# Optimization experiments

Hardware: AMD Instinct MI355X
Metric: run time of the kernel (lower is better)

## Reference

```python
import jax, jax.numpy as jnp
import numpy as np

N, E = 50000, 800000
IN_F, HID, OUT_F, K = 128, 128, 64, 3
LAMBDA_MAX = 2.0  # standard upper bound for normalized-Laplacian eigenvalues (dgl.laplacian_lambda_max)
BN_EPS = 1e-5


def setup_inputs() -> dict:
    key = jax.random.key(0)
    ks = jax.random.split(key, 8)
    s = 0.05
    features = jax.random.normal(ks[0], (N, IN_F), jnp.float32)
    src = jax.random.randint(ks[1], (E,), 0, N)
    dst = jax.random.randint(ks[2], (E,), 0, N)
    W1 = jax.random.normal(ks[3], (HID, K * IN_F), jnp.float32) * s
    b1 = jnp.zeros((HID,), jnp.float32)
    W3 = jax.random.normal(ks[4], (HID, K * HID), jnp.float32) * s
    b3 = jnp.zeros((HID,), jnp.float32)
    gamma = jnp.ones((HID,), jnp.float32)
    beta = jnp.zeros((HID,), jnp.float32)
    Wm1 = jax.random.normal(ks[5], (HID, HID), jnp.float32) * s
    bm1 = jnp.zeros((HID,), jnp.float32)
    Wm2 = jax.random.normal(ks[6], (OUT_F, HID), jnp.float32) * s
    bm2 = jnp.zeros((OUT_F,), jnp.float32)
    return dict(features=features, src=src, dst=dst, W1=W1, b1=b1, W3=W3, b3=b3,
                gamma=gamma, beta=beta, Wm1=Wm1, bm1=bm1, Wm2=Wm2, bm2=bm2)


def chebconv(feat, src, dst, d_invsqrt, W, b, k):
    """DGL ChebConv: T_0 = X, T_1 = Lhat X, T_i = 2 Lhat T_{i-1} - T_{i-2};
    Lhat = (2/lam) (I - Ahat) - I, Ahat = D^{-1/2} A D^{-1/2}; linear over concat of orders."""
    re_norm = 2.0 / LAMBDA_MAX
    n = feat.shape[0]

    def spmv(x):  # Ahat @ x via edge gather (src) + segment-sum scatter (dst)
        return jax.ops.segment_sum((x * d_invsqrt)[src], dst, num_segments=n) * d_invsqrt

    Xs = [feat]
    if k > 1:
        h = spmv(feat)
        Xs.append(-re_norm * h + feat * (re_norm - 1.0))
    for _ in range(2, k):
        h = spmv(Xs[-1])
        Xs.append(-2.0 * re_norm * h + Xs[-1] * (2.0 * (re_norm - 1.0)) - Xs[-2])
    return jnp.concatenate(Xs, axis=1) @ W.T + b  # [N, k*d] @ [d_out, k*d]^T


def reference(features, src, dst, W1, b1, W3, b3, gamma, beta, Wm1, bm1, Wm2, bm2):
    n = features.shape[0]
    in_deg = jax.ops.segment_sum(jnp.ones((src.shape[0],), jnp.float32), dst, num_segments=n)
    d_invsqrt = (jnp.clip(in_deg, 1.0, None) ** -0.5)[:, None]

    x = jax.nn.relu(chebconv(features, src, dst, d_invsqrt, W1, b1, K))
    # BatchNorm1d (training-mode batch stats, biased variance)
    mu = x.mean(axis=0)
    var = x.var(axis=0)
    x = (x - mu) * jax.lax.rsqrt(var + BN_EPS) * gamma + beta
    # NOTE: the source's Chebyshev early-stopping loop computes cheb2(x) repeatedly but
    # never reassigns `x`, so it is output-inert and omitted (same math).
    x_res = x
    x = jax.nn.relu(chebconv(x, src, dst, d_invsqrt, W3, b3, K))
    x = x + x_res  # dropout in eval mode == identity
    h = jax.nn.relu(x @ Wm1.T + bm1)
    return h @ Wm2.T + bm2
```

## Files before the change

### kernel.cpp

```cpp
#include <hip/hip_runtime.h>
#include <hip/hip_bf16.h>
#include <math.h>

#define NF 128

typedef __bf16 bf16x8 __attribute__((ext_vector_type(8)));
typedef unsigned short ushort8 __attribute__((ext_vector_type(8)));
typedef float f32x4 __attribute__((ext_vector_type(4)));
typedef _Float16 half8 __attribute__((ext_vector_type(8)));
typedef _Float16 half4 __attribute__((ext_vector_type(4)));

static inline int ceil_div(int a, int b) { return (a + b - 1) / b; }

__global__ __launch_bounds__(256) void bucket_hist_kernel(const int* __restrict__ dst,
                                                          int* __restrict__ counts,
                                                          int e, int nblk, int nbuck) {
  __shared__ int h[256];
  int t = threadIdx.x, blk = blockIdx.x;
  h[t] = 0;
  __syncthreads();
  int base = blk * 4096;
#pragma unroll
  for (int k = 0; k < 16; ++k) {
    int i = base + k * 256 + t;
    if (i < e) atomicAdd(&h[dst[i] >> 8], 1);
  }
  __syncthreads();
  for (int b = t; b < nbuck; b += 256) counts[b * nblk + blk] = h[b];
}

__global__ __launch_bounds__(256) void bucket_scan_rows_kernel(int* __restrict__ counts,
                                                               int* __restrict__ btot,
                                                               int nblk) {
  __shared__ int sh[256];
  int b = blockIdx.x, t = threadIdx.x;
  int* row = counts + (size_t)b * nblk;
  int carry = 0;
  for (int base = 0; base < nblk; base += 256) {
    int v = (base + t < nblk) ? row[base + t] : 0;
    sh[t] = v;
    __syncthreads();
    for (int off = 1; off < 256; off <<= 1) {
      int add = (t >= off) ? sh[t - off] : 0;
      __syncthreads();
      sh[t] += add;
      __syncthreads();
    }
    if (base + t < nblk) row[base + t] = carry + sh[t] - v;
    carry += sh[255];
    __syncthreads();
  }
  if (t == 0) btot[b] = carry;
}

__global__ __launch_bounds__(256) void bucket_base_kernel(const int* __restrict__ btot,
                                                          int* __restrict__ bbase,
                                                          int nbuck, int e) {
  __shared__ int sh[256];
  __shared__ int carry;
  int t = threadIdx.x;
  if (t == 0) carry = 0;
  __syncthreads();
  for (int base = 0; base < nbuck; base += 256) {
    int v = (base + t < nbuck) ? btot[base + t] : 0;
    sh[t] = v;
    __syncthreads();
    for (int off = 1; off < 256; off <<= 1) {
      int add = (t >= off) ? sh[t - off] : 0;
      __syncthreads();
      sh[t] += add;
      __syncthreads();
    }
    if (base + t < nbuck) bbase[base + t] = carry + sh[t] - v;
    __syncthreads();
    if (t == 0) carry += sh[255];
    __syncthreads();
  }
  if (t == 0) bbase[nbuck] = e;
}

__global__ __launch_bounds__(256) void bucket_bin_kernel(const int* __restrict__ src,
                                                         const int* __restrict__ dst,
                                                         const int* __restrict__ counts,
                                                         const int* __restrict__ bbase,
                                                         int2* __restrict__ binned,
                                                         int e, int nblk, int nbuck) {
  __shared__ int cur[256];
  int t = threadIdx.x, blk = blockIdx.x;
  for (int b = t; b < nbuck; b += 256) cur[b] = counts[b * nblk + blk] + bbase[b];
  __syncthreads();
  int base = blk * 4096;
#pragma unroll
  for (int k = 0; k < 16; ++k) {
    int i = base + k * 256 + t;
    if (i < e) {
      int d = dst[i];
      int pos = atomicAdd(&cur[d >> 8], 1);
      binned[pos] = make_int2(src[i], d);
    }
  }
}

__global__ __launch_bounds__(256) void bucket_finalize_kernel(const int2* __restrict__ binned,
                                                              const int* __restrict__ bbase,
                                                              int* __restrict__ offsets,
                                                              int* __restrict__ csr,
                                                              float* __restrict__ dinv,
                                                              int n, int e, int nbuck) {
  __shared__ int deg[256];
  __shared__ int offs[256];
  __shared__ int cur[256];
  int b = blockIdx.x, t = threadIdx.x;
  int ebeg = bbase[b];
  int eend = bbase[b + 1];
  deg[t] = 0;
  __syncthreads();
  for (int j = ebeg + t; j < eend; j += 256) atomicAdd(&deg[binned[j].y & 255], 1);
  __syncthreads();
  int v = deg[t];
  offs[t] = v;
  __syncthreads();
  for (int off = 1; off < 256; off <<= 1) {
    int add = (t >= off) ? offs[t - off] : 0;
    __syncthreads();
    offs[t] += add;
    __syncthreads();
  }
  int excl = offs[t] - v;
  cur[t] = excl;
  int node = b * 256 + t;
  if (node < n) {
    offsets[node] = ebeg + excl;
    float d = (float)(v > 1 ? v : 1);
    dinv[node] = rsqrtf(d);
  }
  if (b == nbuck - 1 && t == 0) offsets[n] = e;
  __syncthreads();
  for (int j = ebeg + t; j < eend; j += 256) {
    int2 pr = binned[j];
    int pos = atomicAdd(&cur[pr.y & 255], 1);
    csr[ebeg + pos] = pr.x;
  }
}

__device__ __forceinline__ void split8(const float* xv, ushort8& hi, ushort8& lo) {
#pragma unroll
  for (int j = 0; j < 8; ++j) {
    __bf16 hh = (__bf16)xv[j];
    __bf16 ll = (__bf16)(xv[j] - (float)hh);
    hi[j] = __builtin_bit_cast(unsigned short, hh);
    lo[j] = __builtin_bit_cast(unsigned short, ll);
  }
}

__global__ void prep_feat_kernel(const float* __restrict__ feat, const float* __restrict__ dinv,
                                 unsigned short* __restrict__ Fsp, _Float16* __restrict__ xs,
                                 int n) {
  int i = blockIdx.x * 256 + threadIdx.x;
  if (i >= n * 16) return;
  int row = i >> 4, fc = i & 15;
  const float4* s = (const float4*)(feat + (size_t)row * NF + fc * 8);
  float4 a = s[0], b = s[1];
  float xv[8] = {a.x, a.y, a.z, a.w, b.x, b.y, b.z, b.w};
  float d = dinv[row];
  half8 h;
#pragma unroll
  for (int j = 0; j < 8; ++j) h[j] = (_Float16)(xv[j] * d);
  *(half8*)(xs + (size_t)row * NF + fc * 8) = h;
  ushort8 hi, lo;
  split8(xv, hi, lo);
  int swz = (fc ^ (row & 15)) * 8;
  *(ushort8*)(Fsp + (size_t)row * 256 + swz) = hi;
  *(ushort8*)(Fsp + (size_t)row * 256 + 128 + swz) = lo;
}

__global__ __launch_bounds__(256) void spmv_kernel(
    const _Float16* __restrict__ xs16, const float* __restrict__ dinv,
    const int* __restrict__ offsets, const int* __restrict__ csr,
    const float* __restrict__ z, float a, float bz,
    unsigned short* __restrict__ outsp, _Float16* __restrict__ outs16, int n) {
  int w = threadIdx.x >> 6, lane = threadIdx.x & 63;
  int node = blockIdx.x * 4 + w;
  if (node >= n) return;
  int beg = __builtin_amdgcn_readfirstlane(offsets[node]);
  int end = __builtin_amdgcn_readfirstlane(offsets[node + 1]);
  int eh = lane >> 4;
  int cq = lane & 15;

  float acc[8];
#pragma unroll
  for (int j = 0; j < 8; ++j) acc[j] = 0.f;

  int e2 = beg;
  for (; e2 + 8 <= end; e2 += 8) {
    int s0 = csr[e2 + eh];
    int s1 = csr[e2 + 4 + eh];
    half8 g0 = ((const half8*)(xs16 + (size_t)s0 * NF))[cq];
    half8 g1 = ((const half8*)(xs16 + (size_t)s1 * NF))[cq];
#pragma unroll
    for (int j = 0; j < 8; ++j) acc[j] += (float)g0[j];
#pragma unroll
    for (int j = 0; j < 8; ++j) acc[j] += (float)g1[j];
  }
  for (; e2 + 4 <= end; e2 += 4) {
    int s0 = csr[e2 + eh];
    half8 g0 = ((const half8*)(xs16 + (size_t)s0 * NF))[cq];
#pragma unroll
    for (int j = 0; j < 8; ++j) acc[j] += (float)g0[j];
  }
  int rem = end - e2;
  if (eh < rem) {
    int s0 = csr[e2 + eh];
    half8 g0 = ((const half8*)(xs16 + (size_t)s0 * NF))[cq];
#pragma unroll
    for (int j = 0; j < 8; ++j) acc[j] += (float)g0[j];
  }
#pragma unroll
  for (int j = 0; j < 8; ++j) {
    acc[j] += __shfl_xor(acc[j], 16);
    acc[j] += __shfl_xor(acc[j], 32);
  }
  if (eh == 0) {
    float dv = dinv[node];
    float v[8];
#pragma unroll
    for (int j = 0; j < 8; ++j) v[j] = a * dv * acc[j];
    if (z) {
      const f32x4* zp = (const f32x4*)(z + (size_t)node * NF + cq * 8);
      f32x4 z0 = zp[0], z1 = zp[1];
#pragma unroll
      for (int j = 0; j < 4; ++j) { v[j] += bz * z0[j]; v[4 + j] += bz * z1[j]; }
    }
    ushort8 hi, lo;
    split8(v, hi, lo);
    int swz = (cq ^ (node & 15)) * 8;
    *(ushort8*)(outsp + (size_t)node * 256 + swz) = hi;
    *(ushort8*)(outsp + (size_t)node * 256 + 128 + swz) = lo;
    if (outs16) {
      half8 hv;
#pragma unroll
      for (int j = 0; j < 8; ++j) hv[j] = (_Float16)(v[j] * dv);
      *(half8*)(outs16 + (size_t)node * NF + cq * 8) = hv;
    }
  }
}

__device__ __forceinline__ void pack_one(const float* __restrict__ W, ushort8* __restrict__ Wp,
                                         int f, int NT, int K) {
  int lane = f & 63;
  int hl = (f >> 6) & 1;
  int rest = f >> 7;
  int nt = rest % NT;
  int kunit = rest / NT;
  int nrow = nt * 16 + (lane & 15);
  int k0 = kunit * 32 + (lane >> 4) * 8;
  const float* srcp = W + (size_t)nrow * K + k0;
  ushort8 v;
#pragma unroll
  for (int j = 0; j < 8; ++j) {
    float x = srcp[j];
    __bf16 h = (__bf16)x;
    if (hl) h = (__bf16)(x - (float)h);
    v[j] = __builtin_bit_cast(unsigned short, h);
  }
  Wp[f] = v;
}

__global__ void pack_all_kernel(const float* __restrict__ W1, ushort8* __restrict__ P1,
                                const float* __restrict__ W3, ushort8* __restrict__ P3,
                                const float* __restrict__ Wm1, ushort8* __restrict__ PM1,
                                const float* __restrict__ Wm2, ushort8* __restrict__ PM2) {
  int f = blockIdx.x * 256 + threadIdx.x;
  if (f < 12288) pack_one(W1, P1, f, 8, 384);
  else if (f < 24576) pack_one(W3, P3, f - 12288, 8, 384);
  else if (f < 28672) pack_one(Wm1, PM1, f - 24576, 8, 128);
  else if (f < 30720) pack_one(Wm2, PM2, f - 28672, 4, 128);
}


__device__ __forceinline__ void stage_sp(const unsigned short* gsrc, float4* lbuf, int tid) {
  const char* g = (const char*)gsrc;
  char* l = (char*)lbuf;
#pragma unroll
  for (int k = 0; k < 4; ++k) {
    int off = k * 8192 + tid * 16;
    __builtin_amdgcn_global_load_lds(
        (const __attribute__((address_space(1))) void*)(g + off),
        (__attribute__((address_space(3))) void*)(l + off), 16, 0, 0);
  }
}

__device__ __forceinline__ void lds_put_split(unsigned short* L, int row, int col, float v) {
  __bf16 hh = (__bf16)v;
  __bf16 ll = (__bf16)(v - (float)hh);
  int base = row * 256 + (((col >> 3) ^ (row & 15)) << 3) + (col & 7);
  L[base] = __builtin_bit_cast(unsigned short, hh);
  L[base + 128] = __builtin_bit_cast(unsigned short, ll);
}

struct Bchunk {
  ushort8 h[2][2];
  ushort8 l[2][2];
};

__device__ __forceinline__ void loadB(const ushort8* __restrict__ Wp, int kunit0,
                                      int lane, int wn, Bchunk& c) {
#pragma unroll
  for (int k2 = 0; k2 < 2; ++k2) {
#pragma unroll
    for (int j = 0; j < 2; ++j) {
      const ushort8* bp = Wp + (size_t)((kunit0 + k2) * 8 + wn * 2 + j) * 128 + lane;
      c.h[k2][j] = bp[0];
      c.l[k2][j] = bp[64];
    }
  }
}

__device__ __forceinline__ void mfma_chunk(const float4* B4, const Bchunk& c, int kbase,
                                           int lane, int wm, f32x4 (*acc)[2]) {
#pragma unroll
  for (int k2 = 0; k2 < 2; ++k2) {
    int kunit = kbase + k2;
    bf16x8 ah[2], al[2];
#pragma unroll
    for (int mt = 0; mt < 2; ++mt) {
      int arow = wm * 32 + mt * 16 + (lane & 15);
      int fc = (kunit & 3) * 4 + (lane >> 4);
      int idx = arow * 32 + (fc ^ (arow & 15));
      ah[mt] = __builtin_bit_cast(bf16x8, B4[idx]);
      al[mt] = __builtin_bit_cast(bf16x8, B4[idx + 16]);
    }
#pragma unroll
    for (int j = 0; j < 2; ++j) {
      bf16x8 bh = __builtin_bit_cast(bf16x8, c.h[k2][j]);
      bf16x8 bl = __builtin_bit_cast(bf16x8, c.l[k2][j]);
#pragma unroll
      for (int mt = 0; mt < 2; ++mt) {
        acc[mt][j] = __builtin_amdgcn_mfma_f32_16x16x32_bf16(ah[mt], bh, acc[mt][j], 0, 0, 0);
        acc[mt][j] = __builtin_amdgcn_mfma_f32_16x16x32_bf16(ah[mt], bl, acc[mt][j], 0, 0, 0);
        acc[mt][j] = __builtin_amdgcn_mfma_f32_16x16x32_bf16(al[mt], bh, acc[mt][j], 0, 0, 0);
      }
    }
  }
}

template<int NT, int NT2>
__device__ __forceinline__ void gemm_step512(const float4* B4, const ushort8* __restrict__ Wp,
                                             int kunit, int lane, int wm, int wn,
                                             f32x4 (*acc)[NT2]) {
  bf16x8 ah[2], al[2];
#pragma unroll
  for (int mt = 0; mt < 2; ++mt) {
    int arow = wm * 32 + mt * 16 + (lane & 15);
    int fc = (kunit & 3) * 4 + (lane >> 4);
    int idx = arow * 32 + (fc ^ (arow & 15));
    ah[mt] = __builtin_bit_cast(bf16x8, B4[idx]);
    al[mt] = __builtin_bit_cast(bf16x8, B4[idx + 16]);
  }
#pragma unroll
  for (int j = 0; j < NT2; ++j) {
    int nt = wn * NT2 + j;
    const ushort8* bp = Wp + (size_t)(kunit * NT + nt) * 2 * 64 + lane;
    bf16x8 bh = __builtin_bit_cast(bf16x8, bp[0]);
    bf16x8 bl = __builtin_bit_cast(bf16x8, bp[64]);
#pragma unroll
    for (int mt = 0; mt < 2; ++mt) {
      acc[mt][j] = __builtin_amdgcn_mfma_f32_16x16x32_bf16(ah[mt], bh, acc[mt][j], 0, 0, 0);
      acc[mt][j] = __builtin_amdgcn_mfma_f32_16x16x32_bf16(ah[mt], bl, acc[mt][j], 0, 0, 0);
      acc[mt][j] = __builtin_amdgcn_mfma_f32_16x16x32_bf16(al[mt], bh, acc[mt][j], 0, 0, 0);
    }
  }
}

__device__ __forceinline__ void gemm3_pipeline(const unsigned short* A0, const unsigned short* A1,
                                               const unsigned short* A2, const ushort8* Wp,
                                               float4 (*buf)[2048], size_t r0,
                                               int tid, int lane, int wm, int wn,
                                               f32x4 (*acc)[2]) {
  const unsigned short* Aarr[3] = {A0, A1, A2};
  stage_sp(A0 + r0 * 256, buf[0], tid);
  Bchunk bc0, bc1;
#pragma unroll
  for (int p = 0; p < 3; ++p) {
    loadB(Wp, p * 4, lane, wn, bc0);
    if (p + 1 < 3) {
      stage_sp(Aarr[p + 1] + r0 * 256, buf[(p + 1) & 1], tid);
      asm volatile("s_waitcnt vmcnt(12)" ::: "memory");
    } else {
      asm volatile("s_waitcnt vmcnt(8)" ::: "memory");
    }
    __builtin_amdgcn_s_barrier();
    __builtin_amdgcn_sched_barrier(0);
    loadB(Wp, p * 4 + 2, lane, wn, bc1);
    mfma_chunk(buf[p & 1], bc0, p * 4, lane, wm, acc);
    mfma_chunk(buf[p & 1], bc1, p * 4 + 2, lane, wm, acc);
    __builtin_amdgcn_sched_barrier(0);
    __builtin_amdgcn_s_barrier();
  }
}

__global__ __launch_bounds__(512, 4) void conv1_gemm_kernel(
    const unsigned short* __restrict__ A0, const unsigned short* __restrict__ A1,
    const unsigned short* __restrict__ A2,
    const ushort8* __restrict__ Wp, const float* __restrict__ bias,
    float* __restrict__ out, float* __restrict__ stats, int n) {
  __shared__ float4 buf[2][2048];
  __shared__ float sstat[256];

  int tid = threadIdx.x;
  int lane = tid & 63, wid = tid >> 6;
  int wm = wid >> 2, wn = wid & 3;
  size_t r0 = (size_t)blockIdx.x * 64;

  f32x4 acc[2][2];
#pragma unroll
  for (int mt = 0; mt < 2; ++mt)
#pragma unroll
    for (int j = 0; j < 2; ++j) acc[mt][j] = (f32x4)0.f;

  gemm3_pipeline(A0, A1, A2, Wp, buf, r0, tid, lane, wm, wn, acc);

  if (tid < 256) sstat[tid] = 0.f;
  __syncthreads();
#pragma unroll
  for (int mt = 0; mt < 2; ++mt) {
    int rbase = (int)r0 + wm * 32 + mt * 16 + (lane >> 4) * 4;
#pragma unroll
    for (int j = 0; j < 2; ++j) {
      int col = wn * 32 + j * 16 + (lane & 15);
      float b = bias[col];
      float sj = 0.f, qj = 0.f;
#pragma unroll
      for (int i = 0; i < 4; ++i) {
        int row = rbase + i;
        if (row < n) {
          float v = fmaxf(acc[mt][j][i] + b, 0.f);
          out[(size_t)row * NF + col] = v;
          sj += v; qj += v * v;
        }
      }
      sj += __shfl_xor(sj, 16); sj += __shfl_xor(sj, 32);
      qj += __shfl_xor(qj, 16); qj += __shfl_xor(qj, 32);
      if ((lane >> 4) == 0) {
        atomicAdd(&sstat[col], sj);
        atomicAdd(&sstat[128 + col], qj);
      }
    }
  }
  __syncthreads();
  if (tid < 256) atomicAdd(&stats[tid], sstat[tid]);
}

__global__ __launch_bounds__(512, 4) void fused_tail_kernel(
    const unsigned short* __restrict__ Xsp, const unsigned short* __restrict__ T1sp,
    const unsigned short* __restrict__ T2sp, const float* __restrict__ X,
    const ushort8* __restrict__ Wp3, const float* __restrict__ b3,
    const ushort8* __restrict__ WpM1, const float* __restrict__ bm1,
    const ushort8* __restrict__ WpM2, const float* __restrict__ bm2,
    float* __restrict__ out, int n) {
  __shared__ float4 buf[2][2048];
  unsigned short* L = (unsigned short*)buf[0];

  int tid = threadIdx.x;
  int lane = tid & 63, wid = tid >> 6;
  int wm = wid >> 2, wn = wid & 3;
  size_t r0 = (size_t)blockIdx.x * 64;

  f32x4 acc[2][2];
#pragma unroll
  for (int mt = 0; mt < 2; ++mt)
#pragma unroll
    for (int j = 0; j < 2; ++j) acc[mt][j] = (f32x4)0.f;

  gemm3_pipeline(Xsp, T1sp, T2sp, Wp3, buf, r0, tid, lane, wm, wn, acc);

#pragma unroll
  for (int mt = 0; mt < 2; ++mt) {
    int rb = wm * 32 + mt * 16 + (lane >> 4) * 4;
#pragma unroll
    for (int j = 0; j < 2; ++j) {
      int col = wn * 32 + j * 16 + (lane & 15);
      float b = b3[col];
#pragma unroll
      for (int i = 0; i < 4; ++i) {
        int lrow = rb + i;
        int row = (int)r0 + lrow;
        float v = 0.f;
        if (row < n) v = fmaxf(acc[mt][j][i] + b, 0.f) + X[(size_t)row * NF + col];
        lds_put_split(L, lrow, col, v);
      }
    }
  }
  __syncthreads();
  f32x4 acc2[2][2];
#pragma unroll
  for (int mt = 0; mt < 2; ++mt)
#pragma unroll
    for (int j = 0; j < 2; ++j) acc2[mt][j] = (f32x4)0.f;
#pragma unroll
  for (int ks = 0; ks < 4; ++ks)
    gemm_step512<8, 2>(buf[0], WpM1, ks, lane, wm, wn, acc2);
  __syncthreads();
#pragma unroll
  for (int mt = 0; mt < 2; ++mt) {
    int rb = wm * 32 + mt * 16 + (lane >> 4) * 4;
#pragma unroll
    for (int j = 0; j < 2; ++j) {
      int col = wn * 32 + j * 16 + (lane & 15);
      float b = bm1[col];
#pragma unroll
      for (int i = 0; i < 4; ++i) {
        float v = fmaxf(acc2[mt][j][i] + b, 0.f);
        lds_put_split(L, rb + i, col, v);
      }
    }
  }
  __syncthreads();
  f32x4 acc3[2][1];
#pragma unroll
  for (int mt = 0; mt < 2; ++mt) acc3[mt][0] = (f32x4)0.f;
#pragma unroll
  for (int ks = 0; ks < 4; ++ks)
    gemm_step512<4, 1>(buf[0], WpM2, ks, lane, wm, wn, acc3);
#pragma unroll
  for (int mt = 0; mt < 2; ++mt) {
    int rb = wm * 32 + mt * 16 + (lane >> 4) * 4;
    int col = wn * 16 + (lane & 15);
    float b = bm2[col];
#pragma unroll
    for (int i = 0; i < 4; ++i) {
      int row = (int)r0 + rb + i;
      if (row < n) out[(size_t)row * 64 + col] = acc3[mt][0][i] + b;
    }
  }
}

__global__ void bn_apply_kernel(float* __restrict__ x, const float* __restrict__ stats,
                                const float* __restrict__ gamma, const float* __restrict__ beta,
                                const float* __restrict__ dinv,
                                unsigned short* __restrict__ Xsp, _Float16* __restrict__ xs16,
                                float fn, int n) {
  int i = blockIdx.x * 256 + threadIdx.x;
  if (i >= n * 16) return;
  int row = i >> 4, fc = i & 15;
  float4* xp = (float4*)(x + (size_t)row * NF + fc * 8);
  float4 a = xp[0], b = xp[1];
  float xv[8] = {a.x, a.y, a.z, a.w, b.x, b.y, b.z, b.w};
  int c0 = fc * 8;
#pragma unroll
  for (int j = 0; j < 8; ++j) {
    int c = c0 + j;
    float mu = stats[c] / fn;
    float var = stats[NF + c] / fn - mu * mu;
    float s = gamma[c] * rsqrtf(var + 1e-5f);
    xv[j] = (xv[j] - mu) * s + beta[c];
  }
  float4 o0, o1;
  o0.x = xv[0]; o0.y = xv[1]; o0.z = xv[2]; o0.w = xv[3];
  o1.x = xv[4]; o1.y = xv[5]; o1.z = xv[6]; o1.w = xv[7];
  xp[0] = o0; xp[1] = o1;
  float d = dinv[row];
  half8 h;
#pragma unroll
  for (int j = 0; j < 8; ++j) h[j] = (_Float16)(xv[j] * d);
  *(half8*)(xs16 + (size_t)row * NF + fc * 8) = h;
  ushort8 hi, lo;
  split8(xv, hi, lo);
  int swz = (fc ^ (row & 15)) * 8;
  *(ushort8*)(Xsp + (size_t)row * 256 + swz) = hi;
  *(ushort8*)(Xsp + (size_t)row * 256 + 128 + swz) = lo;
}

extern "C" void kernel_launch(void* const* d_in, const int* in_sizes, int n_in,
                              void* d_out, int out_size, void* d_ws, size_t ws_size,
                              hipStream_t stream) {
  const float* feat  = (const float*)d_in[0];
  const int*   src   = (const int*)d_in[1];
  const int*   dst   = (const int*)d_in[2];
  const float* W1    = (const float*)d_in[3];
  const float* b1    = (const float*)d_in[4];
  const float* W3    = (const float*)d_in[5];
  const float* b3    = (const float*)d_in[6];
  const float* gamma = (const float*)d_in[7];
  const float* beta  = (const float*)d_in[8];
  const float* Wm1   = (const float*)d_in[9];
  const float* bm1   = (const float*)d_in[10];
  const float* Wm2   = (const float*)d_in[11];
  const float* bm2   = (const float*)d_in[12];
  int n = in_sizes[0] / NF;
  int e = in_sizes[1];

  char* p = (char*)d_ws;
  auto alloc = [&](size_t bytes) {
    char* r = p;
    p += (bytes + 255) & ~size_t(255);
    return r;
  };
  int nblk  = ceil_div(e, 4096);
  int nbuck = ceil_div(n, 256);

  float* dinv     = (float*)alloc((size_t)n * 4);
  int*   offsets  = (int*)alloc((size_t)(n + 1) * 4);
  int*   counts   = (int*)alloc((size_t)nblk * nbuck * 4);
  int*   btot     = (int*)alloc((size_t)nbuck * 4);
  int*   bbase    = (int*)alloc((size_t)(nbuck + 1) * 4);
  int*   csr      = (int*)alloc((size_t)e * 4);
  float* stats    = (float*)alloc(256 * 4);
  ushort8* Wp1  = (ushort8*)alloc(12 * 8 * 2 * 64 * 16);
  ushort8* Wp3  = (ushort8*)alloc(12 * 8 * 2 * 64 * 16);
  ushort8* WpM1 = (ushort8*)alloc(4 * 8 * 2 * 64 * 16);
  ushort8* WpM2 = (ushort8*)alloc(4 * 4 * 2 * 64 * 16);
  size_t spb = (size_t)(n + 64) * 512;
  unsigned short* Fsp  = (unsigned short*)alloc(spb);
  unsigned short* T1sp = (unsigned short*)alloc(spb);
  unsigned short* T2sp = (unsigned short*)alloc(spb);
  unsigned short* Xsp  = (unsigned short*)alloc(spb);
  float* X = (float*)alloc((size_t)n * NF * 4);
  _Float16* xsA = (_Float16*)alloc((size_t)n * NF * 2);
  _Float16* xsB = (_Float16*)alloc((size_t)n * NF * 2);
  int2* binned = (int2*)Fsp;

  hipMemsetAsync(stats, 0, 256 * 4, stream);

  int fb = ceil_div(n * 16, 256);
  int sb = ceil_div(n, 4);
  int gb = ceil_div(n, 64);

  bucket_hist_kernel<<<nblk, 256, 0, stream>>>(dst, counts, e, nblk, nbuck);
  bucket_scan_rows_kernel<<<nbuck, 256, 0, stream>>>(counts, btot, nblk);
  bucket_base_kernel<<<1, 256, 0, stream>>>(btot, bbase, nbuck, e);
  bucket_bin_kernel<<<nblk, 256, 0, stream>>>(src, dst, counts, bbase, binned, e, nblk, nbuck);
  bucket_finalize_kernel<<<nbuck, 256, 0, stream>>>(binned, bbase, offsets, csr, dinv, n, e, nbuck);

  pack_all_kernel<<<120, 256, 0, stream>>>(W1, Wp1, W3, Wp3, Wm1, WpM1, Wm2, WpM2);

  prep_feat_kernel<<<fb, 256, 0, stream>>>(feat, dinv, Fsp, xsA, n);
  spmv_kernel<<<sb, 256, 0, stream>>>(xsA, dinv, offsets, csr, nullptr, -1.f, 0.f, T1sp, xsB, n);
  spmv_kernel<<<sb, 256, 0, stream>>>(xsB, dinv, offsets, csr, feat, -2.f, -1.f, T2sp, nullptr, n);
  conv1_gemm_kernel<<<gb, 512, 0, stream>>>(Fsp, T1sp, T2sp, Wp1, b1, X, stats, n);

  bn_apply_kernel<<<fb, 256, 0, stream>>>(X, stats, gamma, beta, dinv, Xsp, xsA, (float)n, n);

  spmv_kernel<<<sb, 256, 0, stream>>>(xsA, dinv, offsets, csr, nullptr, -1.f, 0.f, T1sp, xsB, n);
  spmv_kernel<<<sb, 256, 0, stream>>>(xsB, dinv, offsets, csr, X, -2.f, -1.f, T2sp, nullptr, n);

  fused_tail_kernel<<<gb, 512, 0, stream>>>(Xsp, T1sp, T2sp, X, Wp3, b3, WpM1, bm1, WpM2, bm2,
                                            (float*)d_out, n);
}
```

Baseline: 297.3 us.

## Switch activations from split bf16 hi/lo to single fp16 with fp16 intermediates

Activation operands (features, T1, T2, BN output) are stored as one fp16 value instead of a bf16 hi+lo pair. GEMMs drop from three MFMAs per tile to two (A times split-fp16 weights), and LDS staging and global buffers are halved. The conv1 output and residual are kept in fp16; the residual is rebuilt from the dinv-scaled fp16 copy times sqrt(deg), which removes the fp32 X read/write traffic. The cost is lower activation precision (fp16 mantissa, plus an extra rounding from the scaled-copy residual), which adds accuracy risk.

```diff
diff --git a/kernel.cpp b/kernel.cpp
--- a/kernel.cpp
+++ b/kernel.cpp
@@ -4,11 +4,9 @@
 
 #define NF 128
 
-typedef __bf16 bf16x8 __attribute__((ext_vector_type(8)));
 typedef unsigned short ushort8 __attribute__((ext_vector_type(8)));
 typedef float f32x4 __attribute__((ext_vector_type(4)));
 typedef _Float16 half8 __attribute__((ext_vector_type(8)));
-typedef _Float16 half4 __attribute__((ext_vector_type(4)));
 
 static inline int ceil_div(int a, int b) { return (a + b - 1) / b; }
 
@@ -106,6 +104,7 @@
                                                               int* __restrict__ offsets,
                                                               int* __restrict__ csr,
                                                               float* __restrict__ dinv,
+                                                              float* __restrict__ dsq,
                                                               int n, int e, int nbuck) {
   __shared__ int deg[256];
   __shared__ int offs[256];
@@ -133,6 +132,7 @@
     offsets[node] = ebeg + excl;
     float d = (float)(v > 1 ? v : 1);
     dinv[node] = rsqrtf(d);
+    dsq[node] = sqrtf(d);
   }
   if (b == nbuck - 1 && t == 0) offsets[n] = e;
   __syncthreads();
@@ -143,18 +143,9 @@
   }
 }
 
-__device__ __forceinline__ void split8(const float* xv, ushort8& hi, ushort8& lo) {
-#pragma unroll
-  for (int j = 0; j < 8; ++j) {
-    __bf16 hh = (__bf16)xv[j];
-    __bf16 ll = (__bf16)(xv[j] - (float)hh);
-    hi[j] = __builtin_bit_cast(unsigned short, hh);
-    lo[j] = __builtin_bit_cast(unsigned short, ll);
-  }
-}
 
 __global__ void prep_feat_kernel(const float* __restrict__ feat, const float* __restrict__ dinv,
-                                 unsigned short* __restrict__ Fsp, _Float16* __restrict__ xs,
+                                 _Float16* __restrict__ Fsp, _Float16* __restrict__ xs,
                                  int n) {
   int i = blockIdx.x * 256 + threadIdx.x;
   if (i >= n * 16) return;
@@ -163,22 +154,19 @@
   float4 a = s[0], b = s[1];
   float xv[8] = {a.x, a.y, a.z, a.w, b.x, b.y, b.z, b.w};
   float d = dinv[row];
-  half8 h;
-#pragma unroll
-  for (int j = 0; j < 8; ++j) h[j] = (_Float16)(xv[j] * d);
+  half8 h, f;
+#pragma unroll
+  for (int j = 0; j < 8; ++j) { h[j] = (_Float16)(xv[j] * d); f[j] = (_Float16)xv[j]; }
   *(half8*)(xs + (size_t)row * NF + fc * 8) = h;
-  ushort8 hi, lo;
-  split8(xv, hi, lo);
   int swz = (fc ^ (row & 15)) * 8;
-  *(ushort8*)(Fsp + (size_t)row * 256 + swz) = hi;
-  *(ushort8*)(Fsp + (size_t)row * 256 + 128 + swz) = lo;
+  *(half8*)(Fsp + (size_t)row * 128 + swz) = f;
 }
 
 __global__ __launch_bounds__(256) void spmv_kernel(
     const _Float16* __restrict__ xs16, const float* __restrict__ dinv,
     const int* __restrict__ offsets, const int* __restrict__ csr,
-    const float* __restrict__ z, float a, float bz,
-    unsigned short* __restrict__ outsp, _Float16* __restrict__ outs16, int n) {
+    const _Float16* __restrict__ zs16, const float* __restrict__ dsq, float a, float bz,
+    _Float16* __restrict__ outsp, _Float16* __restrict__ outs16, int n) {
   int w = threadIdx.x >> 6, lane = threadIdx.x & 63;
   int node = blockIdx.x * 4 + w;
   if (node >= n) return;
@@ -225,23 +213,18 @@
     float v[8];
 #pragma unroll
     for (int j = 0; j < 8; ++j) v[j] = a * dv * acc[j];
-    if (z) {
-      const f32x4* zp = (const f32x4*)(z + (size_t)node * NF + cq * 8);
-      f32x4 z0 = zp[0], z1 = zp[1];
-#pragma unroll
-      for (int j = 0; j < 4; ++j) { v[j] += bz * z0[j]; v[4 + j] += bz * z1[j]; }
-    }
-    ushort8 hi, lo;
-    split8(v, hi, lo);
+    if (zs16) {
+      float zf = bz * dsq[node];
+      half8 zz = ((const half8*)(zs16 + (size_t)node * NF))[cq];
+#pragma unroll
+      for (int j = 0; j < 8; ++j) v[j] += zf * (float)zz[j];
+    }
+    half8 ho, hs;
+#pragma unroll
+    for (int j = 0; j < 8; ++j) { ho[j] = (_Float16)v[j]; hs[j] = (_Float16)(v[j] * dv); }
     int swz = (cq ^ (node & 15)) * 8;
-    *(ushort8*)(outsp + (size_t)node * 256 + swz) = hi;
-    *(ushort8*)(outsp + (size_t)node * 256 + 128 + swz) = lo;
-    if (outs16) {
-      half8 hv;
-#pragma unroll
-      for (int j = 0; j < 8; ++j) hv[j] = (_Float16)(v[j] * dv);
-      *(half8*)(outs16 + (size_t)node * NF + cq * 8) = hv;
-    }
+    *(half8*)(outsp + (size_t)node * 128 + swz) = ho;
+    if (outs16) *(half8*)(outs16 + (size_t)node * NF + cq * 8) = hs;
   }
 }
 
@@ -259,8 +242,8 @@
 #pragma unroll
   for (int j = 0; j < 8; ++j) {
     float x = srcp[j];
-    __bf16 h = (__bf16)x;
-    if (hl) h = (__bf16)(x - (float)h);
+    _Float16 h = (_Float16)x;
+    if (hl) h = (_Float16)(x - (float)h);
     v[j] = __builtin_bit_cast(unsigned short, h);
   }
   Wp[f] = v;
@@ -278,11 +261,11 @@
 }
 
 
-__device__ __forceinline__ void stage_sp(const unsigned short* gsrc, float4* lbuf, int tid) {
+__device__ __forceinline__ void stage_sp(const _Float16* gsrc, float4* lbuf, int tid) {
   const char* g = (const char*)gsrc;
   char* l = (char*)lbuf;
 #pragma unroll
-  for (int k = 0; k < 4; ++k) {
+  for (int k = 0; k < 2; ++k) {
     int off = k * 8192 + tid * 16;
     __builtin_amdgcn_global_load_lds(
         (const __attribute__((address_space(1))) void*)(g + off),
@@ -290,12 +273,8 @@
   }
 }
 
-__device__ __forceinline__ void lds_put_split(unsigned short* L, int row, int col, float v) {
-  __bf16 hh = (__bf16)v;
-  __bf16 ll = (__bf16)(v - (float)hh);
-  int base = row * 256 + (((col >> 3) ^ (row & 15)) << 3) + (col & 7);
-  L[base] = __builtin_bit_cast(unsigned short, hh);
-  L[base + 128] = __builtin_bit_cast(unsigned short, ll);
+__device__ __forceinline__ void lds_put16(_Float16* L, int row, int col, float v) {
+  L[row * 128 + (((col >> 3) ^ (row & 15)) << 3) + (col & 7)] = (_Float16)v;
 }
 
 struct Bchunk {
@@ -316,76 +295,70 @@
   }
 }
 
-__device__ __forceinline__ void mfma_chunk(const float4* B4, const Bchunk& c, int kbase,
+__device__ __forceinline__ void mfma_chunk(const float4* A4, const Bchunk& c, int kbase,
                                            int lane, int wm, f32x4 (*acc)[2]) {
 #pragma unroll
   for (int k2 = 0; k2 < 2; ++k2) {
     int kunit = kbase + k2;
-    bf16x8 ah[2], al[2];
+    half8 a[2];
 #pragma unroll
     for (int mt = 0; mt < 2; ++mt) {
       int arow = wm * 32 + mt * 16 + (lane & 15);
       int fc = (kunit & 3) * 4 + (lane >> 4);
-      int idx = arow * 32 + (fc ^ (arow & 15));
-      ah[mt] = __builtin_bit_cast(bf16x8, B4[idx]);
-      al[mt] = __builtin_bit_cast(bf16x8, B4[idx + 16]);
+      a[mt] = __builtin_bit_cast(half8, A4[arow * 16 + (fc ^ (arow & 15))]);
     }
 #pragma unroll
     for (int j = 0; j < 2; ++j) {
-      bf16x8 bh = __builtin_bit_cast(bf16x8, c.h[k2][j]);
-      bf16x8 bl = __builtin_bit_cast(bf16x8, c.l[k2][j]);
+      half8 bh = __builtin_bit_cast(half8, c.h[k2][j]);
+      half8 bl = __builtin_bit_cast(half8, c.l[k2][j]);
 #pragma unroll
       for (int mt = 0; mt < 2; ++mt) {
-        acc[mt][j] = __builtin_amdgcn_mfma_f32_16x16x32_bf16(ah[mt], bh, acc[mt][j], 0, 0, 0);
-        acc[mt][j] = __builtin_amdgcn_mfma_f32_16x16x32_bf16(ah[mt], bl, acc[mt][j], 0, 0, 0);
-        acc[mt][j] = __builtin_amdgcn_mfma_f32_16x16x32_bf16(al[mt], bh, acc[mt][j], 0, 0, 0);
+        acc[mt][j] = __builtin_amdgcn_mfma_f32_16x16x32_f16(a[mt], bh, acc[mt][j], 0, 0, 0);
+        acc[mt][j] = __builtin_amdgcn_mfma_f32_16x16x32_f16(a[mt], bl, acc[mt][j], 0, 0, 0);
       }
     }
   }
 }
 
 template<int NT, int NT2>
-__device__ __forceinline__ void gemm_step512(const float4* B4, const ushort8* __restrict__ Wp,
-                                             int kunit, int lane, int wm, int wn,
-                                             f32x4 (*acc)[NT2]) {
-  bf16x8 ah[2], al[2];
+__device__ __forceinline__ void gemm_step16(const float4* A4, const ushort8* __restrict__ Wp,
+                                            int kunit, int lane, int wm, int wn,
+                                            f32x4 (*acc)[NT2]) {
+  half8 a[2];
 #pragma unroll
   for (int mt = 0; mt < 2; ++mt) {
     int arow = wm * 32 + mt * 16 + (lane & 15);
     int fc = (kunit & 3) * 4 + (lane >> 4);
-    int idx = arow * 32 + (fc ^ (arow & 15));
-    ah[mt] = __builtin_bit_cast(bf16x8, B4[idx]);
-    al[mt] = __builtin_bit_cast(bf16x8, B4[idx + 16]);
+    a[mt] = __builtin_bit_cast(half8, A4[arow * 16 + (fc ^ (arow & 15))]);
   }
 #pragma unroll
   for (int j = 0; j < NT2; ++j) {
     int nt = wn * NT2 + j;
     const ushort8* bp = Wp + (size_t)(kunit * NT + nt) * 2 * 64 + lane;
-    bf16x8 bh = __builtin_bit_cast(bf16x8, bp[0]);
-    bf16x8 bl = __builtin_bit_cast(bf16x8, bp[64]);
+    half8 bh = __builtin_bit_cast(half8, bp[0]);
+    half8 bl = __builtin_bit_cast(half8, bp[64]);
 #pragma unroll
     for (int mt = 0; mt < 2; ++mt) {
-      acc[mt][j] = __builtin_amdgcn_mfma_f32_16x16x32_bf16(ah[mt], bh, acc[mt][j], 0, 0, 0);
-      acc[mt][j] = __builtin_amdgcn_mfma_f32_16x16x32_bf16(ah[mt], bl, acc[mt][j], 0, 0, 0);
-      acc[mt][j] = __builtin_amdgcn_mfma_f32_16x16x32_bf16(al[mt], bh, acc[mt][j], 0, 0, 0);
-    }
-  }
-}
-
-__device__ __forceinline__ void gemm3_pipeline(const unsigned short* A0, const unsigned short* A1,
-                                               const unsigned short* A2, const ushort8* Wp,
-                                               float4 (*buf)[2048], size_t r0,
+      acc[mt][j] = __builtin_amdgcn_mfma_f32_16x16x32_f16(a[mt], bh, acc[mt][j], 0, 0, 0);
+      acc[mt][j] = __builtin_amdgcn_mfma_f32_16x16x32_f16(a[mt], bl, acc[mt][j], 0, 0, 0);
+    }
+  }
+}
+
+__device__ __forceinline__ void gemm3_pipeline(const _Float16* A0, const _Float16* A1,
+                                               const _Float16* A2, const ushort8* Wp,
+                                               float4 (*buf)[1024], size_t r0,
                                                int tid, int lane, int wm, int wn,
                                                f32x4 (*acc)[2]) {
-  const unsigned short* Aarr[3] = {A0, A1, A2};
-  stage_sp(A0 + r0 * 256, buf[0], tid);
+  const _Float16* Aarr[3] = {A0, A1, A2};
+  stage_sp(A0 + r0 * 128, buf[0], tid);
   Bchunk bc0, bc1;
 #pragma unroll
   for (int p = 0; p < 3; ++p) {
     loadB(Wp, p * 4, lane, wn, bc0);
     if (p + 1 < 3) {
-      stage_sp(Aarr[p + 1] + r0 * 256, buf[(p + 1) & 1], tid);
-      asm volatile("s_waitcnt vmcnt(12)" ::: "memory");
+      stage_sp(Aarr[p + 1] + r0 * 128, buf[(p + 1) & 1], tid);
+      asm volatile("s_waitcnt vmcnt(10)" ::: "memory");
     } else {
       asm volatile("s_waitcnt vmcnt(8)" ::: "memory");
     }
@@ -400,11 +373,11 @@
 }
 
 __global__ __launch_bounds__(512, 4) void conv1_gemm_kernel(
-    const unsigned short* __restrict__ A0, const unsigned short* __restrict__ A1,
-    const unsigned short* __restrict__ A2,
+    const _Float16* __restrict__ A0, const _Float16* __restrict__ A1,
+    const _Float16* __restrict__ A2,
     const ushort8* __restrict__ Wp, const float* __restrict__ bias,
-    float* __restrict__ out, float* __restrict__ stats, int n) {
-  __shared__ float4 buf[2][2048];
+    _Float16* __restrict__ Xh, float* __restrict__ stats, int n) {
+  __shared__ float4 buf[2][1024];
   __shared__ float sstat[256];
 
   int tid = threadIdx.x;
@@ -435,7 +408,7 @@
         int row = rbase + i;
         if (row < n) {
           float v = fmaxf(acc[mt][j][i] + b, 0.f);
-          out[(size_t)row * NF + col] = v;
+          Xh[(size_t)row * NF + col] = (_Float16)v;
           sj += v; qj += v * v;
         }
       }
@@ -452,14 +425,15 @@
 }
 
 __global__ __launch_bounds__(512, 4) void fused_tail_kernel(
-    const unsigned short* __restrict__ Xsp, const unsigned short* __restrict__ T1sp,
-    const unsigned short* __restrict__ T2sp, const float* __restrict__ X,
+    const _Float16* __restrict__ Xsp, const _Float16* __restrict__ T1sp,
+    const _Float16* __restrict__ T2sp,
+    const _Float16* __restrict__ xsA, const float* __restrict__ dsq,
     const ushort8* __restrict__ Wp3, const float* __restrict__ b3,
     const ushort8* __restrict__ WpM1, const float* __restrict__ bm1,
     const ushort8* __restrict__ WpM2, const float* __restrict__ bm2,
     float* __restrict__ out, int n) {
-  __shared__ float4 buf[2][2048];
-  unsigned short* L = (unsigned short*)buf[0];
+  __shared__ float4 buf[2][1024];
+  _Float16* L = (_Float16*)buf[0];
 
   int tid = threadIdx.x;
   int lane = tid & 63, wid = tid >> 6;
@@ -486,8 +460,11 @@
         int lrow = rb + i;
         int row = (int)r0 + lrow;
         float v = 0.f;
-        if (row < n) v = fmaxf(acc[mt][j][i] + b, 0.f) + X[(size_t)row * NF + col];
-        lds_put_split(L, lrow, col, v);
+        if (row < n) {
+          float xres = (float)xsA[(size_t)row * NF + col] * dsq[row];
+          v = fmaxf(acc[mt][j][i] + b, 0.f) + xres;
+        }
+        lds_put16(L, lrow, col, v);
       }
     }
   }
@@ -499,7 +476,7 @@
     for (int j = 0; j < 2; ++j) acc2[mt][j] = (f32x4)0.f;
 #pragma unroll
   for (int ks = 0; ks < 4; ++ks)
-    gemm_step512<8, 2>(buf[0], WpM1, ks, lane, wm, wn, acc2);
+    gemm_step16<8, 2>(buf[0], WpM1, ks, lane, wm, wn, acc2);
   __syncthreads();
 #pragma unroll
   for (int mt = 0; mt < 2; ++mt) {
@@ -511,7 +488,7 @@
 #pragma unroll
       for (int i = 0; i < 4; ++i) {
         float v = fmaxf(acc2[mt][j][i] + b, 0.f);
-        lds_put_split(L, rb + i, col, v);
+        lds_put16(L, rb + i, col, v);
       }
     }
   }
@@ -521,7 +498,7 @@
   for (int mt = 0; mt < 2; ++mt) acc3[mt][0] = (f32x4)0.f;
 #pragma unroll
   for (int ks = 0; ks < 4; ++ks)
-    gemm_step512<4, 1>(buf[0], WpM2, ks, lane, wm, wn, acc3);
+    gemm_step16<4, 1>(buf[0], WpM2, ks, lane, wm, wn, acc3);
 #pragma unroll
   for (int mt = 0; mt < 2; ++mt) {
     int rb = wm * 32 + mt * 16 + (lane >> 4) * 4;
@@ -535,17 +512,16 @@
   }
 }
 
-__global__ void bn_apply_kernel(float* __restrict__ x, const float* __restrict__ stats,
+__global__ void bn_apply_kernel(const _Float16* __restrict__ Xh, const float* __restrict__ stats,
                                 const float* __restrict__ gamma, const float* __restrict__ beta,
                                 const float* __restrict__ dinv,
-                                unsigned short* __restrict__ Xsp, _Float16* __restrict__ xs16,
+                                _Float16* __restrict__ Xsp, _Float16* __restrict__ xs16,
                                 float fn, int n) {
   int i = blockIdx.x * 256 + threadIdx.x;
   if (i >= n * 16) return;
   int row = i >> 4, fc = i & 15;
-  float4* xp = (float4*)(x + (size_t)row * NF + fc * 8);
-  float4 a = xp[0], b = xp[1];
-  float xv[8] = {a.x, a.y, a.z, a.w, b.x, b.y, b.z, b.w};
+  half8 xh = *(const half8*)(Xh + (size_t)row * NF + fc * 8);
+  float xv[8];
   int c0 = fc * 8;
 #pragma unroll
   for (int j = 0; j < 8; ++j) {
@@ -553,22 +529,15 @@
     float mu = stats[c] / fn;
     float var = stats[NF + c] / fn - mu * mu;
     float s = gamma[c] * rsqrtf(var + 1e-5f);
-    xv[j] = (xv[j] - mu) * s + beta[c];
-  }
-  float4 o0, o1;
-  o0.x = xv[0]; o0.y = xv[1]; o0.z = xv[2]; o0.w = xv[3];
-  o1.x = xv[4]; o1.y = xv[5]; o1.z = xv[6]; o1.w = xv[7];
-  xp[0] = o0; xp[1] = o1;
+    xv[j] = ((float)xh[j] - mu) * s + beta[c];
+  }
   float d = dinv[row];
-  half8 h;
-#pragma unroll
-  for (int j = 0; j < 8; ++j) h[j] = (_Float16)(xv[j] * d);
-  *(half8*)(xs16 + (size_t)row * NF + fc * 8) = h;
-  ushort8 hi, lo;
-  split8(xv, hi, lo);
+  half8 hs, hu;
+#pragma unroll
+  for (int j = 0; j < 8; ++j) { hs[j] = (_Float16)(xv[j] * d); hu[j] = (_Float16)xv[j]; }
+  *(half8*)(xs16 + (size_t)row * NF + fc * 8) = hs;
   int swz = (fc ^ (row & 15)) * 8;
-  *(ushort8*)(Xsp + (size_t)row * 256 + swz) = hi;
-  *(ushort8*)(Xsp + (size_t)row * 256 + 128 + swz) = lo;
+  *(half8*)(Xsp + (size_t)row * 128 + swz) = hu;
 }
 
 extern "C" void kernel_launch(void* const* d_in, const int* in_sizes, int n_in,
@@ -600,6 +569,7 @@
   int nbuck = ceil_div(n, 256);
 
   float* dinv     = (float*)alloc((size_t)n * 4);
+  float* dsq      = (float*)alloc((size_t)n * 4);
   int*   offsets  = (int*)alloc((size_t)(n + 1) * 4);
   int*   counts   = (int*)alloc((size_t)nblk * nbuck * 4);
   int*   btot     = (int*)alloc((size_t)nbuck * 4);
@@ -610,14 +580,14 @@
   ushort8* Wp3  = (ushort8*)alloc(12 * 8 * 2 * 64 * 16);
   ushort8* WpM1 = (ushort8*)alloc(4 * 8 * 2 * 64 * 16);
   ushort8* WpM2 = (ushort8*)alloc(4 * 4 * 2 * 64 * 16);
-  size_t spb = (size_t)(n + 64) * 512;
-  unsigned short* Fsp  = (unsigned short*)alloc(spb);
-  unsigned short* T1sp = (unsigned short*)alloc(spb);
-  unsigned short* T2sp = (unsigned short*)alloc(spb);
-  unsigned short* Xsp  = (unsigned short*)alloc(spb);
-  float* X = (float*)alloc((size_t)n * NF * 4);
-  _Float16* xsA = (_Float16*)alloc((size_t)n * NF * 2);
-  _Float16* xsB = (_Float16*)alloc((size_t)n * NF * 2);
+  size_t spb = (size_t)(n + 64) * 256;
+  _Float16* Fsp  = (_Float16*)alloc(spb);
+  _Float16* T1sp = (_Float16*)alloc(spb);
+  _Float16* T2sp = (_Float16*)alloc(spb);
+  _Float16* Xsp  = (_Float16*)alloc(spb);
+  _Float16* Xh   = (_Float16*)alloc((size_t)n * NF * 2);
+  _Float16* xsA  = (_Float16*)alloc((size_t)n * NF * 2);
+  _Float16* xsB  = (_Float16*)alloc((size_t)n * NF * 2);
   int2* binned = (int2*)Fsp;
 
   hipMemsetAsync(stats, 0, 256 * 4, stream);
@@ -630,20 +600,20 @@
   bucket_scan_rows_kernel<<<nbuck, 256, 0, stream>>>(counts, btot, nblk);
   bucket_base_kernel<<<1, 256, 0, stream>>>(btot, bbase, nbuck, e);
   bucket_bin_kernel<<<nblk, 256, 0, stream>>>(src, dst, counts, bbase, binned, e, nblk, nbuck);
-  bucket_finalize_kernel<<<nbuck, 256, 0, stream>>>(binned, bbase, offsets, csr, dinv, n, e, nbuck);
+  bucket_finalize_kernel<<<nbuck, 256, 0, stream>>>(binned, bbase, offsets, csr, dinv, dsq, n, e, nbuck);
 
   pack_all_kernel<<<120, 256, 0, stream>>>(W1, Wp1, W3, Wp3, Wm1, WpM1, Wm2, WpM2);
 
   prep_feat_kernel<<<fb, 256, 0, stream>>>(feat, dinv, Fsp, xsA, n);
-  spmv_kernel<<<sb, 256, 0, stream>>>(xsA, dinv, offsets, csr, nullptr, -1.f, 0.f, T1sp, xsB, n);
-  spmv_kernel<<<sb, 256, 0, stream>>>(xsB, dinv, offsets, csr, feat, -2.f, -1.f, T2sp, nullptr, n);
-  conv1_gemm_kernel<<<gb, 512, 0, stream>>>(Fsp, T1sp, T2sp, Wp1, b1, X, stats, n);
-
-  bn_apply_kernel<<<fb, 256, 0, stream>>>(X, stats, gamma, beta, dinv, Xsp, xsA, (float)n, n);
-
-  spmv_kernel<<<sb, 256, 0, stream>>>(xsA, dinv, offsets, csr, nullptr, -1.f, 0.f, T1sp, xsB, n);
-  spmv_kernel<<<sb, 256, 0, stream>>>(xsB, dinv, offsets, csr, X, -2.f, -1.f, T2sp, nullptr, n);
-
-  fused_tail_kernel<<<gb, 512, 0, stream>>>(Xsp, T1sp, T2sp, X, Wp3, b3, WpM1, bm1, WpM2, bm2,
-                                            (float*)d_out, n);
-}
+  spmv_kernel<<<sb, 256, 0, stream>>>(xsA, dinv, offsets, csr, nullptr, nullptr, -1.f, 0.f, T1sp, xsB, n);
+  spmv_kernel<<<sb, 256, 0, stream>>>(xsB, dinv, offsets, csr, xsA, dsq, -2.f, -1.f, T2sp, nullptr, n);
+  conv1_gemm_kernel<<<gb, 512, 0, stream>>>(Fsp, T1sp, T2sp, Wp1, b1, Xh, stats, n);
+
+  bn_apply_kernel<<<fb, 256, 0, stream>>>(Xh, stats, gamma, beta, dinv, Xsp, xsA, (float)n, n);
+
+  spmv_kernel<<<sb, 256, 0, stream>>>(xsA, dinv, offsets, csr, nullptr, nullptr, -1.f, 0.f, T1sp, xsB, n);
+  spmv_kernel<<<sb, 256, 0, stream>>>(xsB, dinv, offsets, csr, xsA, dsq, -2.f, -1.f, T2sp, nullptr, n);
+
+  fused_tail_kernel<<<gb, 512, 0, stream>>>(Xsp, T1sp, T2sp, xsA, dsq, Wp3, b3, WpM1, bm1,
+                                            WpM2, bm2, (float*)d_out, n);
+}
```

Measured after the change: 271.7 us. 8.6% less time.
